# Optimization experiments

Hardware: AMD Instinct MI355X
Metric: run time of the kernel (lower is better)

Reference implementation:

```python
import jax, jax.numpy as jnp
import numpy as np

N_NODES = 4096  # nodes per graph (output1 reshaped to [-1, N_NODES])


def setup_inputs() -> dict:
    key = jax.random.key(0)
    ks = jax.random.split(key, 10)
    total_nodes = 64 * N_NODES          # 64 graphs of 4096 nodes
    n_edges = total_nodes * 8           # avg degree 8 lattice-like graph
    n_hidden = 128
    return {
        "node_features": jax.random.normal(ks[0], (total_nodes, 1), jnp.float32),
        "src": jax.random.randint(ks[1], (n_edges,), 0, total_nodes, jnp.int32),
        "dst": jax.random.randint(ks[2], (n_edges,), 0, total_nodes, jnp.int32),
        "w_self1": jax.random.normal(ks[3], (1, n_hidden), jnp.float32) * 0.5,
        "w_neigh1": jax.random.normal(ks[4], (1, n_hidden), jnp.float32) * 0.5,
        "b1": jnp.zeros((n_hidden,), jnp.float32),
        "w_self2": jax.random.normal(ks[5], (n_hidden, 1), jnp.float32) * (1.0 / np.sqrt(n_hidden)),
        "w_neigh2": jax.random.normal(ks[6], (n_hidden, 1), jnp.float32) * (1.0 / np.sqrt(n_hidden)),
        "b2": jnp.zeros((1,), jnp.float32),
        "w3": jax.random.normal(ks[7], (N_NODES, N_NODES), jnp.float32) * (1.0 / np.sqrt(N_NODES)),
        "b3": jnp.zeros((N_NODES,), jnp.float32),
    }


def _sage_mean(feat, src, dst, w_self, w_neigh, b, num_nodes):
    # gather source-node features along edges, mean-reduce at destination
    agg = jax.ops.segment_sum(feat[src], dst, num_segments=num_nodes)
    deg = jax.ops.segment_sum(jnp.ones((src.shape[0], 1), feat.dtype), dst,
                              num_segments=num_nodes)
    h_neigh = agg / jnp.maximum(deg, 1.0)
    return feat @ w_self + h_neigh @ w_neigh + b


def reference(node_features, src, dst, w_self1, w_neigh1, b1,
              w_self2, w_neigh2, b2, w3, b3):
    n = node_features.shape[0]
    h1 = jnp.tanh(_sage_mean(node_features, src, dst, w_self1, w_neigh1, b1, n))
    out1 = _sage_mean(h1, src, dst, w_self2, w_neigh2, b2, n)
    output1 = out1.reshape(-1, N_NODES)          # [batch, n_nodes]
    h2 = jnp.tanh(output1)
    output2 = h2 @ w3 + b3
    return (output1, output2)
```

## Files before the change

kernel.cpp:

```cpp
#include <hip/hip_runtime.h>


#define NTOT (64 * 4096)
#define NHID 128
#define GK   4096
#define KCH  256
#define KCHUNKS 16
#define NBINS 1024
#define BSZ   256
#define BSH   8
#define CAP   2432
#define SCB   256

typedef unsigned int u32;

__device__ __forceinline__ float fast_tanh(float x) {
    float ax = fabsf(x);
    float t  = __expf(-2.0f * ax);
    float r  = (1.0f - t) * __builtin_amdgcn_rcpf(1.0f + t);
    return copysignf(r, x);
}


__global__ void __launch_bounds__(1024) scatter_x(const int* __restrict__ src,
                                                  const int* __restrict__ dst,
                                                  int n_edges,
                                                  int* __restrict__ edge_cnt,
                                                  u32* __restrict__ packed) {
    __shared__ int lc[NBINS];
    __shared__ int lbase[NBINS];
    int t = threadIdx.x;
    lc[t] = 0;
    __syncthreads();
    int per = (n_edges + gridDim.x - 1) / gridDim.x;
    int e0 = blockIdx.x * per;
    int e1 = min(e0 + per, n_edges);

    int dreg[8], sreg[8];
#pragma unroll
    for (int i = 0; i < 8; ++i) {
        int e = e0 + t + i * 1024;
        bool ok = e < e1;
        int d = ok ? dst[e] : -1;
        dreg[i] = d;
        sreg[i] = ok ? src[e] : 0;
        if (ok) atomicAdd(&lc[d >> BSH], 1);
    }
    __syncthreads();
    lbase[t] = atomicAdd(&edge_cnt[t], lc[t]);
    lc[t] = 0;
    __syncthreads();
#pragma unroll
    for (int i = 0; i < 8; ++i) {
        int d = dreg[i];
        if (d >= 0) {
            int b = d >> BSH;
            int pos = lbase[b] + atomicAdd(&lc[b], 1);
            if (pos < CAP)
                packed[(size_t)b * CAP + pos] =
                    ((u32)(d & (BSZ - 1)) << 18) | (u32)sreg[i];
        }
    }
}

__global__ void __launch_bounds__(256) agn1_x(const u32* __restrict__ packed,
                                              const int* __restrict__ edge_cnt,
                                              const float* __restrict__ nf,
                                              const float* __restrict__ w_s1,
                                              const float* __restrict__ w_n1,
                                              const float* __restrict__ bb1,
                                              const float* __restrict__ w_s2,
                                              const float* __restrict__ w_n2,
                                              float* __restrict__ degf,
                                              float* __restrict__ selfp,
                                              float* __restrict__ sp) {
    __shared__ float lsum[BSZ];
    __shared__ float lcnt[BSZ];
    __shared__ float lws1[NHID], lwn1[NHID], lb1[NHID], lws2[NHID], lwn2[NHID];
    int t = threadIdx.x;
    int b = blockIdx.x;
    lsum[t] = 0.0f;
    lcnt[t] = 0.0f;
    if (t < NHID) {
        lws1[t] = w_s1[t];
        lwn1[t] = w_n1[t];
        lb1[t]  = bb1[t];
        lws2[t] = w_s2[t];
        lwn2[t] = w_n2[t];
    }
    __syncthreads();
    int en = min(edge_cnt[b], CAP);
    const u32* pk = packed + (size_t)b * CAP;
    for (int e = t; e < en; e += 256) {
        u32 p = pk[e];
        int local = (int)(p >> 18);
        atomicAdd(&lsum[local], nf[p & 0x3FFFFu]);
        atomicAdd(&lcnt[local], 1.0f);
    }
    __syncthreads();
    int v = b * BSZ + t;
    float cf = lcnt[t];
    float hn = lsum[t] / fmaxf(cf, 1.0f);
    float f  = nf[v];
    float a = 0.0f, s2 = 0.0f;
#pragma unroll 8
    for (int j = 0; j < NHID; ++j) {
        float th = fast_tanh(fmaf(f, lws1[j], fmaf(hn, lwn1[j], lb1[j])));
        a  = fmaf(th, lws2[j], a);
        s2 = fmaf(th, lwn2[j], s2);
    }
    degf[v]  = cf;
    selfp[v] = a;
    sp[v]    = s2;
}

__global__ void __launch_bounds__(256) agn2_x(const u32* __restrict__ packed,
                                              const int* __restrict__ edge_cnt,
                                              const float* __restrict__ spv,
                                              const float* __restrict__ selfp,
                                              const float* __restrict__ degf,
                                              const float* __restrict__ b2p,
                                              float* __restrict__ out1,
                                              float* __restrict__ h2t) {
    __shared__ float lsum[BSZ];
    int t = threadIdx.x;
    int b = blockIdx.x;
    lsum[t] = 0.0f;
    __syncthreads();
    int en = min(edge_cnt[b], CAP);
    const u32* pk = packed + (size_t)b * CAP;
    for (int e = t; e < en; e += 256) {
        u32 p = pk[e];
        atomicAdd(&lsum[p >> 18], spv[p & 0x3FFFFu]);
    }
    __syncthreads();
    int v = b * BSZ + t;
    float o = selfp[v] + lsum[t] / fmaxf(degf[v], 1.0f) + b2p[0];
    out1[v] = o;
    int r = v >> 12;
    int k = v & 4095;
    h2t[k * 64 + r] = fast_tanh(o);
}

__global__ void __launch_bounds__(512, 4) gemm_x(const float* __restrict__ h2t,
                                                 const float* __restrict__ w3,
                                                 float* __restrict__ Cpart) {
    int lane = threadIdx.x & 63;
    int wv   = threadIdx.x >> 6;
    int col  = blockIdx.x * 64 + lane;
    int k0   = blockIdx.y * KCH;
    int row0 = __builtin_amdgcn_readfirstlane(wv * 8);

    const float* Ap = h2t + (size_t)k0 * 64 + row0;
    const float* wp = w3 + (size_t)k0 * GK + col;

    float acc[8];
#pragma unroll
    for (int r = 0; r < 8; ++r) acc[r] = 0.0f;

    float bvA[8], bvB[8];
    float avA[8], avB[8];

#pragma unroll
    for (int j = 0; j < 8; ++j) bvA[j] = wp[(size_t)j * GK];
#pragma unroll
    for (int r = 0; r < 8; ++r) avA[r] = Ap[r];

    for (int kk = 0; kk < KCH; kk += 16) {
#pragma unroll
        for (int j = 0; j < 8; ++j) bvB[j] = wp[(size_t)(kk + 8 + j) * GK];
#pragma unroll
        for (int j = 0; j < 8; ++j) {
            const float* An = Ap + (size_t)(kk + j + 1) * 64;
            if ((j & 1) == 0) {
#pragma unroll
                for (int r = 0; r < 8; ++r) avB[r] = An[r];
                float b = bvA[j];
#pragma unroll
                for (int r = 0; r < 8; ++r) acc[r] = fmaf(avA[r], b, acc[r]);
            } else {
#pragma unroll
                for (int r = 0; r < 8; ++r) avA[r] = An[r];
                float b = bvA[j];
#pragma unroll
                for (int r = 0; r < 8; ++r) acc[r] = fmaf(avB[r], b, acc[r]);
            }
        }
        if (kk + 16 < KCH) {
#pragma unroll
            for (int j = 0; j < 8; ++j) bvA[j] = wp[(size_t)(kk + 16 + j) * GK];
        }
#pragma unroll
        for (int j = 0; j < 8; ++j) {
            int kn = kk + 8 + j + 1;
            if (kn > KCH - 1) kn = KCH - 1;
            const float* An = Ap + (size_t)kn * 64;
            if ((j & 1) == 0) {
#pragma unroll
                for (int r = 0; r < 8; ++r) avB[r] = An[r];
                float b = bvB[j];
#pragma unroll
                for (int r = 0; r < 8; ++r) acc[r] = fmaf(avA[r], b, acc[r]);
            } else {
#pragma unroll
                for (int r = 0; r < 8; ++r) avA[r] = An[r];
                float b = bvB[j];
#pragma unroll
                for (int r = 0; r < 8; ++r) acc[r] = fmaf(avB[r], b, acc[r]);
            }
        }
    }

    float* Cp = Cpart + (size_t)blockIdx.y * NTOT + (size_t)row0 * GK + col;
#pragma unroll
    for (int r = 0; r < 8; ++r) Cp[(size_t)r * GK] = acc[r];
}

__global__ void reduce_x(const float4* __restrict__ Cpart, const float4* __restrict__ b3v,
                         float4* __restrict__ out2) {
    int v = blockIdx.x * blockDim.x + threadIdx.x;
    float4 s = b3v[v & 1023];
#pragma unroll
    for (int kc = 0; kc < KCHUNKS; ++kc) {
        float4 c = Cpart[(size_t)kc * (NTOT / 4) + v];
        s.x += c.x; s.y += c.y; s.z += c.z; s.w += c.w;
    }
    out2[v] = s;
}


__global__ void edge_pass1_f(const int* __restrict__ src, const int* __restrict__ dst,
                             const float* __restrict__ nf, float* __restrict__ agg,
                             float* __restrict__ deg, int n_edges) {
    int e = blockIdx.x * blockDim.x + threadIdx.x;
    if (e >= n_edges) return;
    int s = src[e], d = dst[e];
    atomicAdd(&agg[d], nf[s]);
    atomicAdd(&deg[d], 1.0f);
}

__global__ void node1_f(const float* __restrict__ nf, float* s0,
                        const float* __restrict__ deg,
                        const float* __restrict__ w_s1, const float* __restrict__ w_n1,
                        const float* __restrict__ bb1,
                        const float* __restrict__ w_s2, const float* __restrict__ w_n2,
                        float* __restrict__ sp) {
    __shared__ float lws1[NHID], lwn1[NHID], lb1[NHID], lws2[NHID], lwn2[NHID];
    int tid = threadIdx.x;
    if (tid < NHID) {
        lws1[tid] = w_s1[tid];
        lwn1[tid] = w_n1[tid];
        lb1[tid]  = bb1[tid];
        lws2[tid] = w_s2[tid];
        lwn2[tid] = w_n2[tid];
    }
    __syncthreads();
    int v = blockIdx.x * blockDim.x + tid;
    float f  = nf[v];
    float hn = s0[v] / fmaxf(deg[v], 1.0f);
    float a = 0.0f, s = 0.0f;
#pragma unroll 8
    for (int j = 0; j < NHID; ++j) {
        float t = fast_tanh(fmaf(f, lws1[j], fmaf(hn, lwn1[j], lb1[j])));
        a = fmaf(t, lws2[j], a);
        s = fmaf(t, lwn2[j], s);
    }
    s0[v] = a;
    sp[v] = s;
}

__global__ void edge_pass2_f(const int* __restrict__ src, const int* __restrict__ dst,
                             const float* __restrict__ sp, float* __restrict__ agg2,
                             int n_edges) {
    int e = blockIdx.x * blockDim.x + threadIdx.x;
    if (e >= n_edges) return;
    atomicAdd(&agg2[dst[e]], sp[src[e]]);
}

__global__ void node2_f(const float* __restrict__ s0, const float* __restrict__ agg2,
                        const float* __restrict__ deg, const float* __restrict__ b2p,
                        const float* __restrict__ b3p,
                        float* __restrict__ out1, float* __restrict__ h2t,
                        float* __restrict__ out2) {
    int v = blockIdx.x * blockDim.x + threadIdx.x;
    float o = s0[v] + agg2[v] / fmaxf(deg[v], 1.0f) + b2p[0];
    out1[v] = o;
    int r = v >> 12;
    int k = v & 4095;
    h2t[k * 64 + r] = fast_tanh(o);
    out2[v] = b3p[v & 4095];
}

__global__ void __launch_bounds__(256) gemm_f(const float* __restrict__ h2t,
                                              const float* __restrict__ w3,
                                              float* __restrict__ out2) {
    int n  = blockIdx.x * 256 + threadIdx.x;
    int k0 = blockIdx.y * KCH;
    float acc[64];
#pragma unroll
    for (int r = 0; r < 64; ++r) acc[r] = 0.0f;
    for (int k = k0; k < k0 + KCH; ++k) {
        float bv = w3[(size_t)k * GK + n];
        const float* Ak = h2t + k * 64;
#pragma unroll
        for (int r = 0; r < 64; ++r) acc[r] = fmaf(Ak[r], bv, acc[r]);
    }
#pragma unroll
    for (int r = 0; r < 64; ++r) atomicAdd(&out2[r * GK + n], acc[r]);
}


extern "C" void kernel_launch(void* const* d_in, const int* in_sizes, int n_in,
                              void* d_out, int out_size, void* d_ws, size_t ws_size,
                              hipStream_t stream) {
    const float* nf  = (const float*)d_in[0];
    const int*   src = (const int*)d_in[1];
    const int*   dst = (const int*)d_in[2];
    const float* ws1 = (const float*)d_in[3];
    const float* wn1 = (const float*)d_in[4];
    const float* b1  = (const float*)d_in[5];
    const float* ws2 = (const float*)d_in[6];
    const float* wn2 = (const float*)d_in[7];
    const float* b2  = (const float*)d_in[8];
    const float* w3  = (const float*)d_in[9];
    const float* b3  = (const float*)d_in[10];
    float* out1 = (float*)d_out;
    float* out2 = (float*)d_out + NTOT;

    int n_edges = in_sizes[1];
    int eb = (n_edges + 255) / 256;

    if (ws_size >= (size_t)20 * 1024 * 1024 && n_edges <= (1 << 21)) {
        char*  base     = (char*)d_ws;
        u32*   packed   = (u32*)base;
        float* degf     = (float*)(base + 10485760);
        float* selfp    = (float*)(base + 11534336);
        float* spbuf    = (float*)(base + 12582912);
        float* h2t      = (float*)(base + 16777216);
        int*   edge_cnt = (int*)(base + 17825792);
        float* Cpart    = (float*)base;

        (void)hipMemsetAsync(edge_cnt, 0, NBINS * sizeof(int), stream);
        scatter_x<<<SCB, 1024, 0, stream>>>(src, dst, n_edges, edge_cnt, packed);
        agn1_x<<<NBINS, BSZ, 0, stream>>>(packed, edge_cnt, nf, ws1, wn1, b1,
                                          ws2, wn2, degf, selfp, spbuf);
        agn2_x<<<NBINS, BSZ, 0, stream>>>(packed, edge_cnt, spbuf, selfp, degf,
                                          b2, out1, h2t);
        gemm_x<<<dim3(GK / 64, KCHUNKS), 512, 0, stream>>>(h2t, w3, Cpart);
        reduce_x<<<NTOT / 4 / 256, 256, 0, stream>>>((const float4*)Cpart,
                                                     (const float4*)b3, (float4*)out2);
    } else {
        float* ws = (float*)d_ws;
        float* S0 = ws;
        float* S1 = ws + 1 * NTOT;
        float* S2 = ws + 2 * NTOT;
        float* S3 = ws + 3 * NTOT;

        (void)hipMemsetAsync(S0, 0, (size_t)3 * NTOT * sizeof(float), stream);
        edge_pass1_f<<<eb, 256, 0, stream>>>(src, dst, nf, S0, S1, n_edges);
        node1_f<<<NTOT / 256, 256, 0, stream>>>(nf, S0, S1, ws1, wn1, b1, ws2, wn2, S3);
        edge_pass2_f<<<eb, 256, 0, stream>>>(src, dst, S3, S2, n_edges);
        node2_f<<<NTOT / 256, 256, 0, stream>>>(S0, S2, S1, b2, b3, out1, S3, out2);
        gemm_f<<<dim3(GK / 256, KCHUNKS), 256, 0, stream>>>(S3, w3, out2);
    }
}
```

Measured before the change: 226.4 us.

## Replace binned edge scatter with direct vectorized global atomic aggregation

Removes the bucket-sort scatter kernel and the LDS-binned aggregation. Edges are now read four at a time via int4 loads, and neighbor sums and degrees are accumulated with global float atomics, followed by simple per-node kernels. This drops the packing pass and its capacity limit, but heavy global atomic traffic to random addresses now goes through L2 twice. Float atomic ordering also makes sums nondeterministic.

```diff
diff --git a/kernel.cpp b/kernel.cpp
--- a/kernel.cpp
+++ b/kernel.cpp
@@ -6,11 +6,6 @@
 #define GK   4096
 #define KCH  256
 #define KCHUNKS 16
-#define NBINS 1024
-#define BSZ   256
-#define BSH   8
-#define CAP   2432
-#define SCB   256
 
 typedef unsigned int u32;
 
@@ -22,65 +17,42 @@
 }
 
 
-__global__ void __launch_bounds__(1024) scatter_x(const int* __restrict__ src,
-                                                  const int* __restrict__ dst,
-                                                  int n_edges,
-                                                  int* __restrict__ edge_cnt,
-                                                  u32* __restrict__ packed) {
-    __shared__ int lc[NBINS];
-    __shared__ int lbase[NBINS];
-    int t = threadIdx.x;
-    lc[t] = 0;
-    __syncthreads();
-    int per = (n_edges + gridDim.x - 1) / gridDim.x;
-    int e0 = blockIdx.x * per;
-    int e1 = min(e0 + per, n_edges);
-
-    int dreg[8], sreg[8];
-#pragma unroll
-    for (int i = 0; i < 8; ++i) {
-        int e = e0 + t + i * 1024;
-        bool ok = e < e1;
-        int d = ok ? dst[e] : -1;
-        dreg[i] = d;
-        sreg[i] = ok ? src[e] : 0;
-        if (ok) atomicAdd(&lc[d >> BSH], 1);
-    }
-    __syncthreads();
-    lbase[t] = atomicAdd(&edge_cnt[t], lc[t]);
-    lc[t] = 0;
-    __syncthreads();
-#pragma unroll
-    for (int i = 0; i < 8; ++i) {
-        int d = dreg[i];
-        if (d >= 0) {
-            int b = d >> BSH;
-            int pos = lbase[b] + atomicAdd(&lc[b], 1);
-            if (pos < CAP)
-                packed[(size_t)b * CAP + pos] =
-                    ((u32)(d & (BSZ - 1)) << 18) | (u32)sreg[i];
-        }
-    }
-}
-
-__global__ void __launch_bounds__(256) agn1_x(const u32* __restrict__ packed,
-                                              const int* __restrict__ edge_cnt,
-                                              const float* __restrict__ nf,
-                                              const float* __restrict__ w_s1,
-                                              const float* __restrict__ w_n1,
-                                              const float* __restrict__ bb1,
-                                              const float* __restrict__ w_s2,
-                                              const float* __restrict__ w_n2,
-                                              float* __restrict__ degf,
-                                              float* __restrict__ selfp,
-                                              float* __restrict__ sp) {
-    __shared__ float lsum[BSZ];
-    __shared__ float lcnt[BSZ];
+__global__ void __launch_bounds__(256) edge1_a(const int4* __restrict__ src4,
+                                               const int4* __restrict__ dst4,
+                                               int n4,
+                                               const float* __restrict__ nf,
+                                               float* __restrict__ agg,
+                                               float* __restrict__ deg) {
+    int i = blockIdx.x * blockDim.x + threadIdx.x;
+    if (i >= n4) return;
+    int4 s = src4[i];
+    int4 d = dst4[i];
+    float g0 = nf[s.x];
+    float g1 = nf[s.y];
+    float g2 = nf[s.z];
+    float g3 = nf[s.w];
+    atomicAdd(&agg[d.x], g0);
+    atomicAdd(&deg[d.x], 1.0f);
+    atomicAdd(&agg[d.y], g1);
+    atomicAdd(&deg[d.y], 1.0f);
+    atomicAdd(&agg[d.z], g2);
+    atomicAdd(&deg[d.z], 1.0f);
+    atomicAdd(&agg[d.w], g3);
+    atomicAdd(&deg[d.w], 1.0f);
+}
+
+__global__ void __launch_bounds__(256) node1_a(const float* __restrict__ nf,
+                                               const float* __restrict__ agg,
+                                               const float* __restrict__ deg,
+                                               const float* __restrict__ w_s1,
+                                               const float* __restrict__ w_n1,
+                                               const float* __restrict__ bb1,
+                                               const float* __restrict__ w_s2,
+                                               const float* __restrict__ w_n2,
+                                               float* __restrict__ selfp,
+                                               float* __restrict__ sp) {
     __shared__ float lws1[NHID], lwn1[NHID], lb1[NHID], lws2[NHID], lwn2[NHID];
     int t = threadIdx.x;
-    int b = blockIdx.x;
-    lsum[t] = 0.0f;
-    lcnt[t] = 0.0f;
     if (t < NHID) {
         lws1[t] = w_s1[t];
         lwn1[t] = w_n1[t];
@@ -89,18 +61,8 @@
         lwn2[t] = w_n2[t];
     }
     __syncthreads();
-    int en = min(edge_cnt[b], CAP);
-    const u32* pk = packed + (size_t)b * CAP;
-    for (int e = t; e < en; e += 256) {
-        u32 p = pk[e];
-        int local = (int)(p >> 18);
-        atomicAdd(&lsum[local], nf[p & 0x3FFFFu]);
-        atomicAdd(&lcnt[local], 1.0f);
-    }
-    __syncthreads();
-    int v = b * BSZ + t;
-    float cf = lcnt[t];
-    float hn = lsum[t] / fmaxf(cf, 1.0f);
+    int v = blockIdx.x * blockDim.x + t;
+    float hn = agg[v] / fmaxf(deg[v], 1.0f);
     float f  = nf[v];
     float a = 0.0f, s2 = 0.0f;
 #pragma unroll 8
@@ -109,33 +71,37 @@
         a  = fmaf(th, lws2[j], a);
         s2 = fmaf(th, lwn2[j], s2);
     }
-    degf[v]  = cf;
     selfp[v] = a;
     sp[v]    = s2;
 }
 
-__global__ void __launch_bounds__(256) agn2_x(const u32* __restrict__ packed,
-                                              const int* __restrict__ edge_cnt,
-                                              const float* __restrict__ spv,
-                                              const float* __restrict__ selfp,
-                                              const float* __restrict__ degf,
-                                              const float* __restrict__ b2p,
-                                              float* __restrict__ out1,
-                                              float* __restrict__ h2t) {
-    __shared__ float lsum[BSZ];
-    int t = threadIdx.x;
-    int b = blockIdx.x;
-    lsum[t] = 0.0f;
-    __syncthreads();
-    int en = min(edge_cnt[b], CAP);
-    const u32* pk = packed + (size_t)b * CAP;
-    for (int e = t; e < en; e += 256) {
-        u32 p = pk[e];
-        atomicAdd(&lsum[p >> 18], spv[p & 0x3FFFFu]);
-    }
-    __syncthreads();
-    int v = b * BSZ + t;
-    float o = selfp[v] + lsum[t] / fmaxf(degf[v], 1.0f) + b2p[0];
+__global__ void __launch_bounds__(256) edge2_a(const int4* __restrict__ src4,
+                                               const int4* __restrict__ dst4,
+                                               int n4,
+                                               const float* __restrict__ spv,
+                                               float* __restrict__ agg2) {
+    int i = blockIdx.x * blockDim.x + threadIdx.x;
+    if (i >= n4) return;
+    int4 s = src4[i];
+    int4 d = dst4[i];
+    float g0 = spv[s.x];
+    float g1 = spv[s.y];
+    float g2 = spv[s.z];
+    float g3 = spv[s.w];
+    atomicAdd(&agg2[d.x], g0);
+    atomicAdd(&agg2[d.y], g1);
+    atomicAdd(&agg2[d.z], g2);
+    atomicAdd(&agg2[d.w], g3);
+}
+
+__global__ void __launch_bounds__(256) node2_a(const float* __restrict__ selfp,
+                                               const float* __restrict__ agg2,
+                                               const float* __restrict__ deg,
+                                               const float* __restrict__ b2p,
+                                               float* __restrict__ out1,
+                                               float* __restrict__ h2t) {
+    int v = blockIdx.x * blockDim.x + threadIdx.x;
+    float o = selfp[v] + agg2[v] / fmaxf(deg[v], 1.0f) + b2p[0];
     out1[v] = o;
     int r = v >> 12;
     int k = v & 4095;
@@ -330,22 +296,27 @@
     int n_edges = in_sizes[1];
     int eb = (n_edges + 255) / 256;
 
-    if (ws_size >= (size_t)20 * 1024 * 1024 && n_edges <= (1 << 21)) {
-        char*  base     = (char*)d_ws;
-        u32*   packed   = (u32*)base;
-        float* degf     = (float*)(base + 10485760);
-        float* selfp    = (float*)(base + 11534336);
-        float* spbuf    = (float*)(base + 12582912);
-        float* h2t      = (float*)(base + 16777216);
-        int*   edge_cnt = (int*)(base + 17825792);
-        float* Cpart    = (float*)base;
-
-        (void)hipMemsetAsync(edge_cnt, 0, NBINS * sizeof(int), stream);
-        scatter_x<<<SCB, 1024, 0, stream>>>(src, dst, n_edges, edge_cnt, packed);
-        agn1_x<<<NBINS, BSZ, 0, stream>>>(packed, edge_cnt, nf, ws1, wn1, b1,
-                                          ws2, wn2, degf, selfp, spbuf);
-        agn2_x<<<NBINS, BSZ, 0, stream>>>(packed, edge_cnt, spbuf, selfp, degf,
-                                          b2, out1, h2t);
+    if (ws_size >= (size_t)20 * 1024 * 1024 && (n_edges & 3) == 0) {
+        char*  base  = (char*)d_ws;
+        float* agg   = (float*)base;
+        float* deg   = (float*)(base + 1048576);
+        float* agg2  = (float*)(base + 2097152);
+        float* selfp = (float*)(base + 3145728);
+        float* sp    = (float*)(base + 4194304);
+        float* h2t   = (float*)(base + 16777216);
+        float* Cpart = (float*)base;
+
+        int n4  = n_edges >> 2;
+        int eb4 = (n4 + 255) / 256;
+
+        (void)hipMemsetAsync(agg, 0, (size_t)3 * 1048576, stream);
+        edge1_a<<<eb4, 256, 0, stream>>>((const int4*)src, (const int4*)dst,
+                                         n4, nf, agg, deg);
+        node1_a<<<NTOT / 256, 256, 0, stream>>>(nf, agg, deg, ws1, wn1, b1,
+                                                ws2, wn2, selfp, sp);
+        edge2_a<<<eb4, 256, 0, stream>>>((const int4*)src, (const int4*)dst,
+                                         n4, sp, agg2);
+        node2_a<<<NTOT / 256, 256, 0, stream>>>(selfp, agg2, deg, b2, out1, h2t);
         gemm_x<<<dim3(GK / 64, KCHUNKS), 512, 0, stream>>>(h2t, w3, Cpart);
         reduce_x<<<NTOT / 4 / 256, 256, 0, stream>>>((const float4*)Cpart,
                                                      (const float4*)b3, (float4*)out2);
```

Result: slower. 487.0 us (+115.1%).
